# Performance work log

Hardware: AMD Instinct MI355X
Metric: run time of the kernel (lower is better)

Reference implementation:

```python
import jax, jax.numpy as jnp
import numpy as np

B, L, C = 4, 2048, 1024
H = 16
D = C // H
MAX_SCALE_MUL = float(np.log(100.0))


def setup_inputs() -> dict:
    key = jax.random.key(0)
    ks = jax.random.split(key, 4)
    x = jax.random.normal(ks[0], (B, L, C), dtype=jnp.float32)
    attn_bias = jnp.zeros((1, 1, L, L), dtype=jnp.float32)
    qkv_w = jax.random.normal(ks[1], (3 * C, C), dtype=jnp.float32) * (C ** -0.5)
    q_bias = jnp.zeros((C,), dtype=jnp.float32)
    v_bias = jnp.zeros((C,), dtype=jnp.float32)
    scale_mul = jnp.full((1, H, 1, 1), np.log(4.0), dtype=jnp.float32)
    proj_w = jax.random.normal(ks[2], (C, C), dtype=jnp.float32) * (C ** -0.5)
    proj_b = jnp.zeros((C,), dtype=jnp.float32)
    return {"x": x, "attn_bias": attn_bias, "qkv_w": qkv_w, "q_bias": q_bias,
            "v_bias": v_bias, "scale_mul": scale_mul, "proj_w": proj_w, "proj_b": proj_b}


def _l2norm(t, eps=1e-12):
    # matches F.normalize(dim=-1): x / max(||x||, eps)
    n = jnp.sqrt(jnp.sum(t * t, axis=-1, keepdims=True))
    return t / jnp.maximum(n, eps)


def reference(x, attn_bias, qkv_w, q_bias, v_bias, scale_mul, proj_w, proj_b):
    zero_k_bias = jnp.zeros_like(q_bias)
    bias = jnp.concatenate([q_bias, zero_k_bias, v_bias])  # [3C]
    qkv = jnp.einsum('blc,oc->blo', x, qkv_w) + bias        # [B,L,3C]
    qkv = qkv.reshape(B, L, 3, H, D).transpose(2, 0, 3, 1, 4)  # [3,B,H,L,D]
    q, k, v = qkv[0], qkv[1], qkv[2]
    sm = jnp.exp(jnp.minimum(scale_mul, MAX_SCALE_MUL))     # [1,H,1,1]
    q = _l2norm(q) * sm
    k = _l2norm(k)
    scores = jnp.einsum('bhqd,bhkd->bhqk', q, k) * 1.0      # scale=1.0 (l2-norm path)
    scores = scores + attn_bias
    probs = jax.nn.softmax(scores, axis=-1)
    out = jnp.einsum('bhqk,bhkd->bhqd', probs, v)           # [B,H,L,D]
    out = out.transpose(0, 2, 1, 3).reshape(B, L, C)
    return jnp.einsum('blc,oc->blo', out, proj_w) + proj_b
```

## Files before the change

### kernel.cpp

```cpp
#include <hip/hip_runtime.h>
#include <cstdint>


typedef __bf16 bfx8 __attribute__((ext_vector_type(8)));
typedef __bf16 bfx4 __attribute__((ext_vector_type(4)));
typedef float  f32x4 __attribute__((ext_vector_type(4)));

#define NB   4
#define NH   16
#define SEQ  2048
#define CH   1024
#define DD   64
#define MROWS (NB*SEQ)
#define BHLD  (NB*NH*SEQ*DD)
#define LOG2E 1.44269504088896340736f

__device__ __forceinline__ void async16(void* lds, const void* g) {
  __builtin_amdgcn_global_load_lds((const __attribute__((address_space(1))) void*)g,
                                   (__attribute__((address_space(3))) void*)lds, 16, 0, 0);
}
__device__ __forceinline__ f32x4 mfma16(bfx8 a, bfx8 b, f32x4 c) {
  return __builtin_amdgcn_mfma_f32_16x16x32_bf16(a, b, c, 0, 0, 0);
}

extern "C" __device__ float __ocml_exp2_f32(float);
__device__ __forceinline__ float fexp2(float x) {
#if __has_builtin(__builtin_amdgcn_exp2f)
  return __builtin_amdgcn_exp2f(x);
#else
  return __ocml_exp2_f32(x);
#endif
}

__global__ __launch_bounds__(256) void cast_kernel(const float4* __restrict__ src,
                                                   __bf16* __restrict__ dst, int n4) {
  int i = blockIdx.x * 256 + threadIdx.x;
  if (i >= n4) return;
  float4 v = src[i];
  float vv[4] = {v.x, v.y, v.z, v.w};
  bfx4 h;
  #pragma unroll
  for (int j = 0; j < 4; ++j) h[j] = (__bf16)vv[j];
  *(bfx4*)(dst + 4*(size_t)i) = h;
}

__global__ __launch_bounds__(256) void split_kernel(const float4* __restrict__ src,
                                                    __bf16* __restrict__ hi,
                                                    __bf16* __restrict__ lo, int n4) {
  int i = blockIdx.x * 256 + threadIdx.x;
  if (i >= n4) return;
  float4 v = src[i];
  float vv[4] = {v.x, v.y, v.z, v.w};
  bfx4 h, l;
  #pragma unroll
  for (int j = 0; j < 4; ++j) {
    __bf16 hb = (__bf16)vv[j];
    h[j] = hb;
    l[j] = (__bf16)(vv[j] - (float)hb);
  }
  *(bfx4*)(hi + 4*(size_t)i) = h;
  *(bfx4*)(lo + 4*(size_t)i) = l;
}

__global__ __launch_bounds__(256) void scan_nz(const uint4* __restrict__ p, int n4,
                                               int* __restrict__ flag) {
  unsigned acc = 0;
  const int stride = gridDim.x * 256;
  for (int i = blockIdx.x * 256 + threadIdx.x; i < n4; i += stride) {
    uint4 u = p[i];
    acc |= (u.x | u.y | u.z | u.w) & 0x7fffffffu;
  }
  if (acc) atomicOr(flag, 1);
}

__global__ __launch_bounds__(256, 2) void gemmq(
    const __bf16* __restrict__ Ag, const __bf16* __restrict__ Bg,
    const int Ntiles, const int K,
    const float* __restrict__ biasA, const float* __restrict__ biasB,
    const float* __restrict__ scale_mul,
    __bf16* __restrict__ outQ, __bf16* __restrict__ outV)
{
  __shared__ alignas(16) char lds[16384];
  const int tid = threadIdx.x;
  const int lane = tid & 63, w = tid >> 6;
  const int l15 = lane & 15, l4 = lane >> 4;
  const int nwg = (int)gridDim.x;
  const int wk = (int)(blockIdx.x & 7) * (nwg >> 3) + (int)(blockIdx.x >> 3);
  const int mt = wk / Ntiles, nt = wk % Ntiles;
  const int m0 = mt * 128, n0 = nt * 128;
  const int wm = (w >> 1) * 64, wn = (w & 1) * 64;

  const f32x4 zz = {0.f, 0.f, 0.f, 0.f};
  f32x4 acc[4][4];
  #pragma unroll
  for (int a = 0; a < 4; ++a)
    #pragma unroll
    for (int b = 0; b < 4; ++b) acc[a][b] = zz;

  int st_row[2], st_c[2], st_lds[2];
  #pragma unroll
  for (int i = 0; i < 2; ++i) {
    const int s = i*256 + tid;
    st_row[i] = s >> 2;
    st_c[i]   = (s & 3) ^ ((st_row[i] >> 1) & 3);
    st_lds[i] = (i*256 + w*64) * 16;
  }

  for (int k0 = 0; k0 < K; k0 += 32) {
    __syncthreads();
    #pragma unroll
    for (int i = 0; i < 2; ++i) {
      const size_t ga = (size_t)(m0 + st_row[i]) * K + (size_t)(k0 + st_c[i]*8);
      const size_t gb = (size_t)(n0 + st_row[i]) * K + (size_t)(k0 + st_c[i]*8);
      async16(lds +        st_lds[i], Ag + ga);
      async16(lds + 8192 + st_lds[i], Bg + gb);
    }
    __syncthreads();

    bfx8 ah[4], bh[4];
    #pragma unroll
    for (int f = 0; f < 4; ++f) {
      const int ra = wm + f*16 + l15;
      ah[f] = *(const bfx8*)(lds + ra*64 + ((l4 ^ ((ra >> 1) & 3)) * 16));
      const int rb = wn + f*16 + l15;
      bh[f] = *(const bfx8*)(lds + 8192 + rb*64 + ((l4 ^ ((rb >> 1) & 3)) * 16));
    }
    __builtin_amdgcn_s_setprio(1);
    #pragma unroll
    for (int mf = 0; mf < 4; ++mf)
      #pragma unroll
      for (int nf = 0; nf < 4; ++nf)
        acc[mf][nf] = mfma16(ah[mf], bh[nf], acc[mf][nf]);
    __builtin_amdgcn_s_setprio(0);
  }

  const int gcb = n0 + wn;
  const int which = gcb >> 10;
  const int hh = (gcb & (CH-1)) >> 6;
  float smul = 1.f;
  if (which == 0) smul = __expf(fminf(scale_mul[hh], 4.605170185988091f)) * LOG2E;
  #pragma unroll
  for (int mf = 0; mf < 4; ++mf)
    #pragma unroll
    for (int rg = 0; rg < 4; ++rg) {
      #pragma unroll
      for (int nf = 0; nf < 4; ++nf) {
        const int gc = gcb + nf*16 + l15;
        acc[mf][nf][rg] += (which == 0) ? biasA[gc]
                         : ((which == 2) ? biasB[gc - 2*CH] : 0.f);
      }
      const int gr = m0 + wm + mf*16 + 4*l4 + rg;
      const int bb = gr >> 11, ll = gr & (SEQ-1);
      float sc = 1.f;
      if (which < 2) {
        float ss = 0.f;
        #pragma unroll
        for (int nf = 0; nf < 4; ++nf) ss += acc[mf][nf][rg] * acc[mf][nf][rg];
        ss += __shfl_xor(ss, 1); ss += __shfl_xor(ss, 2);
        ss += __shfl_xor(ss, 4); ss += __shfl_xor(ss, 8);
        sc = smul / fmaxf(sqrtf(ss), 1e-12f);
      }
      #pragma unroll
      for (int nf = 0; nf < 4; ++nf) {
        const float v = acc[mf][nf][rg] * sc;
        const int dd = nf*16 + l15;
        if (which < 2)
          outQ[(size_t)which*BHLD + ((size_t)((bb*NH + hh)*SEQ) + ll)*DD + dd] = (__bf16)v;
        else
          outV[((size_t)(bb*NH + hh)*DD + dd)*SEQ + ll] = (__bf16)v;
      }
    }
}

__global__ __launch_bounds__(256, 2) void gemm128s(
    const __bf16* __restrict__ Agh, const __bf16* __restrict__ Agl,
    const __bf16* __restrict__ Bgh, const __bf16* __restrict__ Bgl,
    const int Ntiles, const int K,
    const float* __restrict__ biasA, float* __restrict__ outF)
{
  __shared__ alignas(16) char lds[32768];
  const int tid = threadIdx.x;
  const int lane = tid & 63, w = tid >> 6;
  const int l15 = lane & 15, l4 = lane >> 4;
  const int nwg = (int)gridDim.x;
  const int wk = (int)(blockIdx.x & 7) * (nwg >> 3) + (int)(blockIdx.x >> 3);
  const int mt = wk / Ntiles, nt = wk % Ntiles;
  const int m0 = mt * 128, n0 = nt * 128;
  const int wm = (w >> 1) * 64, wn = (w & 1) * 64;

  const f32x4 zz = {0.f, 0.f, 0.f, 0.f};
  f32x4 acc[4][4];
  #pragma unroll
  for (int a = 0; a < 4; ++a)
    #pragma unroll
    for (int b = 0; b < 4; ++b) acc[a][b] = zz;

  int st_row[2], st_c[2], st_lds[2];
  #pragma unroll
  for (int i = 0; i < 2; ++i) {
    const int s = i*256 + tid;
    st_row[i] = s >> 2;
    st_c[i]   = (s & 3) ^ ((st_row[i] >> 1) & 3);
    st_lds[i] = (i*256 + w*64) * 16;
  }

  for (int k0 = 0; k0 < K; k0 += 32) {
    __syncthreads();
    #pragma unroll
    for (int i = 0; i < 2; ++i) {
      const size_t ga = (size_t)(m0 + st_row[i]) * K + (size_t)(k0 + st_c[i]*8);
      const size_t gb = (size_t)(n0 + st_row[i]) * K + (size_t)(k0 + st_c[i]*8);
      async16(lds +         st_lds[i], Agh + ga);
      async16(lds +  8192 + st_lds[i], Agl + ga);
      async16(lds + 16384 + st_lds[i], Bgh + gb);
      async16(lds + 24576 + st_lds[i], Bgl + gb);
    }
    __syncthreads();

    bfx8 ah[4], al[4], bh[4], bl[4];
    #pragma unroll
    for (int f = 0; f < 4; ++f) {
      const int ra = wm + f*16 + l15;
      const int oa = ra*64 + ((l4 ^ ((ra >> 1) & 3)) * 16);
      ah[f] = *(const bfx8*)(lds + oa);
      al[f] = *(const bfx8*)(lds + 8192 + oa);
      const int rb = wn + f*16 + l15;
      const int ob = rb*64 + ((l4 ^ ((rb >> 1) & 3)) * 16);
      bh[f] = *(const bfx8*)(lds + 16384 + ob);
      bl[f] = *(const bfx8*)(lds + 24576 + ob);
    }
    __builtin_amdgcn_s_setprio(1);
    #pragma unroll
    for (int mf = 0; mf < 4; ++mf)
      #pragma unroll
      for (int nf = 0; nf < 4; ++nf) {
        acc[mf][nf] = mfma16(al[mf], bh[nf], acc[mf][nf]);
        acc[mf][nf] = mfma16(ah[mf], bl[nf], acc[mf][nf]);
        acc[mf][nf] = mfma16(ah[mf], bh[nf], acc[mf][nf]);
      }
    __builtin_amdgcn_s_setprio(0);
  }

  #pragma unroll
  for (int mf = 0; mf < 4; ++mf)
    #pragma unroll
    for (int nf = 0; nf < 4; ++nf)
      #pragma unroll
      for (int rg = 0; rg < 4; ++rg) {
        const int gr = m0 + wm + mf*16 + 4*l4 + rg;
        const int gc = n0 + wn + nf*16 + l15;
        outF[(size_t)gr*CH + gc] = acc[mf][nf][rg] + biasA[gc];
      }
}

__global__ __launch_bounds__(256, 2) void attn_kernel(
    const __bf16* __restrict__ qn, const __bf16* __restrict__ kn,
    const __bf16* __restrict__ vtg, const float* __restrict__ scale_mul,
    const float* __restrict__ bias, const int* __restrict__ flag,
    __bf16* __restrict__ ao_hi, __bf16* __restrict__ ao_lo)
{
  __shared__ alignas(16) char Ks[2][8192];
  __shared__ alignas(16) char Vt[2][8192];
  __shared__ alignas(16) char Ps[16384];

  const int tid = threadIdx.x, lane = tid & 63, w = tid >> 6;
  const int l15 = lane & 15, l4 = lane >> 4;
  const int wk = (int)(blockIdx.x & 7) * 128 + (int)(blockIdx.x >> 3);
  const int qt = wk & 15, h = (wk >> 4) & 15, b = wk >> 8;
  const size_t bh = ((size_t)(b*NH + h)) * SEQ * DD;
  const int hasbias = *flag;
  char* Pw = Ps + w*4096;

  const float Mh = __expf(fminf(scale_mul[h], 4.605170185988091f)) * LOG2E * 1.01f;

  bfx8 Qf[2][2];
  const int q0 = qt*128 + w*32;
  #pragma unroll
  for (int mf = 0; mf < 2; ++mf)
    #pragma unroll
    for (int kd = 0; kd < 2; ++kd)
      Qf[mf][kd] = *(const bfx8*)(qn + bh + (size_t)(q0 + mf*16 + l15)*DD + kd*32 + l4*8);

  bfx8 ones;
  #pragma unroll
  for (int j = 0; j < 8; ++j) ones[j] = (__bf16)1.0f;

  const f32x4 zz = {0.f, 0.f, 0.f, 0.f};
  f32x4 O[2][4];
  f32x4 lsum[2] = {zz, zz};
  float m_[2] = {-1e30f, -1e30f}, l_[2] = {0.f, 0.f};
  #pragma unroll
  for (int mf = 0; mf < 2; ++mf)
    #pragma unroll
    for (int nd = 0; nd < 4; ++nd) O[mf][nd] = zz;

  auto stage = [&](int t, int buf) {
    const __bf16* ksrc = kn + bh + (size_t)t*64*DD;
    const __bf16* vsrc = vtg + bh + (size_t)t*64;
    #pragma unroll
    for (int i = 0; i < 2; ++i) {
      const int s = i*256 + tid;
      const int row = s >> 3;
      const int c = (s & 7) ^ (row & 7);
      async16(Ks[buf] + (size_t)(i*256 + w*64)*16, ksrc + (size_t)row*DD + c*8);
      async16(Vt[buf] + (size_t)(i*256 + w*64)*16, vsrc + (size_t)row*SEQ + c*8);
    }
  };

  stage(0, 0);
  asm volatile("s_waitcnt vmcnt(0)" ::: "memory");
  __builtin_amdgcn_s_barrier();

  #pragma unroll 1
  for (int t = 0; t < 32; ++t) {
    const int cur = t & 1;
    if (t + 1 < 32) stage(t + 1, cur ^ 1);

    f32x4 ST[2][4];
    __builtin_amdgcn_s_setprio(1);
    #pragma unroll
    for (int nf = 0; nf < 4; ++nf) {
      const int r = nf*16 + l15;
      const bfx8 K0 = *(const bfx8*)(Ks[cur] + r*128 + ((l4 ^ (r & 7)) * 16));
      const bfx8 K1 = *(const bfx8*)(Ks[cur] + r*128 + (((4 + l4) ^ (r & 7)) * 16));
      #pragma unroll
      for (int mf = 0; mf < 2; ++mf) {
        f32x4 sacc = mfma16(K0, Qf[mf][0], zz);
        ST[mf][nf] = mfma16(K1, Qf[mf][1], sacc);
      }
    }
    __builtin_amdgcn_s_setprio(0);

    if (!hasbias) {
      #pragma unroll
      for (int mf = 0; mf < 2; ++mf) {
        const int row = mf*16 + l15;
        #pragma unroll
        for (int nf = 0; nf < 4; ++nf) {
          bfx4 p4;
          #pragma unroll
          for (int rg = 0; rg < 4; ++rg)
            p4[rg] = (__bf16)fexp2(ST[mf][nf][rg] - Mh);
          const int cpos = (2*nf + (l4 >> 1)) ^ (row & 7);
          *(bfx4*)(Pw + row*128 + cpos*16 + (l4 & 1)*8) = p4;
        }
      }
    } else {
      #pragma unroll
      for (int mf = 0; mf < 2; ++mf) {
        const size_t qg = (size_t)(q0 + mf*16 + l15);
        const float* bp = bias + qg*SEQ + (size_t)t*64;
        #pragma unroll
        for (int nf = 0; nf < 4; ++nf)
          #pragma unroll
          for (int rg = 0; rg < 4; ++rg)
            ST[mf][nf][rg] += bp[nf*16 + 4*l4 + rg] * LOG2E;

        f32x4 mv = ST[mf][0];
        #pragma unroll
        for (int nf = 1; nf < 4; ++nf)
          #pragma unroll
          for (int rg = 0; rg < 4; ++rg) mv[rg] = fmaxf(mv[rg], ST[mf][nf][rg]);
        float mx = fmaxf(fmaxf(mv[0], mv[1]), fmaxf(mv[2], mv[3]));
        mx = fmaxf(mx, __shfl_xor(mx, 16));
        mx = fmaxf(mx, __shfl_xor(mx, 32));
        const bool skip = __all(mx - m_[mf] <= 12.0f) != 0;
        const float mn = skip ? m_[mf] : fmaxf(m_[mf], mx);
        f32x4 sv = zz;
        #pragma unroll
        for (int nf = 0; nf < 4; ++nf)
          #pragma unroll
          for (int rg = 0; rg < 4; ++rg) {
            const float pv = fexp2(ST[mf][nf][rg] - mn);
            ST[mf][nf][rg] = pv;
            sv[rg] += pv;
          }
        float rs = (sv[0] + sv[1]) + (sv[2] + sv[3]);
        rs += __shfl_xor(rs, 16);
        rs += __shfl_xor(rs, 32);
        if (skip) {
          l_[mf] += rs;
        } else {
          const float corr = fexp2(m_[mf] - mn);
          l_[mf] = l_[mf] * corr + rs;
          m_[mf] = mn;
          #pragma unroll
          for (int nd = 0; nd < 4; ++nd)
            #pragma unroll
            for (int rg = 0; rg < 4; ++rg) O[mf][nd][rg] *= corr;
        }
        const int row = mf*16 + l15;
        #pragma unroll
        for (int nf = 0; nf < 4; ++nf) {
          bfx4 p4;
          #pragma unroll
          for (int rg = 0; rg < 4; ++rg) p4[rg] = (__bf16)ST[mf][nf][rg];
          const int cpos = (2*nf + (l4 >> 1)) ^ (row & 7);
          *(bfx4*)(Pw + row*128 + cpos*16 + (l4 & 1)*8) = p4;
        }
      }
    }

    __builtin_amdgcn_s_setprio(1);
    #pragma unroll
    for (int kk = 0; kk < 2; ++kk) {
      bfx8 Pf[2];
      #pragma unroll
      for (int mf = 0; mf < 2; ++mf) {
        const int row = mf*16 + l15;
        Pf[mf] = *(const bfx8*)(Pw + row*128 + (((4*kk + l4) ^ (row & 7)) * 16));
      }
      #pragma unroll
      for (int nd = 0; nd < 4; ++nd) {
        const int dr = nd*16 + l15;
        const bfx8 Vf = *(const bfx8*)(Vt[cur] + dr*128 + (((4*kk + l4) ^ (dr & 7)) * 16));
        #pragma unroll
        for (int mf = 0; mf < 2; ++mf)
          O[mf][nd] = mfma16(Vf, Pf[mf], O[mf][nd]);
      }
      if (!hasbias) {
        lsum[0] = mfma16(ones, Pf[0], lsum[0]);
        lsum[1] = mfma16(ones, Pf[1], lsum[1]);
      }
    }
    __builtin_amdgcn_s_setprio(0);

    asm volatile("s_waitcnt vmcnt(0)" ::: "memory");
    __builtin_amdgcn_s_barrier();
  }

  if (!hasbias) { l_[0] = lsum[0][0]; l_[1] = lsum[1][0]; }

  #pragma unroll
  for (int mf = 0; mf < 2; ++mf) {
    const float inv = 1.f / l_[mf];
    const int qg = q0 + mf*16 + l15;
    #pragma unroll
    for (int nd = 0; nd < 4; ++nd) {
      bfx4 hb, lb;
      #pragma unroll
      for (int rg = 0; rg < 4; ++rg) {
        const float v = O[mf][nd][rg] * inv;
        hb[rg] = (__bf16)v;
        lb[rg] = (__bf16)(v - (float)hb[rg]);
      }
      const size_t idx = ((size_t)(b*SEQ + qg))*CH + h*DD + nd*16 + 4*l4;
      *(bfx4*)(ao_hi + idx) = hb;
      *(bfx4*)(ao_lo + idx) = lb;
    }
  }
}

extern "C" void kernel_launch(void* const* d_in, const int* in_sizes, int n_in,
                              void* d_out, int out_size, void* d_ws, size_t ws_size,
                              hipStream_t stream) {
  const float* x         = (const float*)d_in[0];
  const float* attn_bias = (const float*)d_in[1];
  const float* qkv_w     = (const float*)d_in[2];
  const float* q_bias    = (const float*)d_in[3];
  const float* v_bias    = (const float*)d_in[4];
  const float* scale_mul = (const float*)d_in[5];
  const float* proj_w    = (const float*)d_in[6];
  const float* proj_b    = (const float*)d_in[7];
  float* out = (float*)d_out;

  char* ws = (char*)d_ws;
  size_t off = 0;
  auto alloc = [&](size_t n) { char* p = ws + off; off += (n + 255) & ~(size_t)255; return p; };
  __bf16* x_h  = (__bf16*)alloc((size_t)MROWS*CH*2);
  __bf16* w_h  = (__bf16*)alloc((size_t)3*CH*CH*2);
  __bf16* p_h  = (__bf16*)alloc((size_t)CH*CH*2);
  __bf16* p_l  = (__bf16*)alloc((size_t)CH*CH*2);
  __bf16* qkvn = (__bf16*)alloc((size_t)2*BHLD*2);
  __bf16* vt   = (__bf16*)alloc((size_t)BHLD*2);
  __bf16* ao_h = (__bf16*)alloc((size_t)MROWS*CH*2);
  __bf16* ao_l = (__bf16*)alloc((size_t)MROWS*CH*2);
  int*    flag = (int*)alloc(256);

  cast_kernel<<<MROWS*CH/4/256, 256, 0, stream>>>((const float4*)x, x_h, MROWS*CH/4);
  cast_kernel<<<3*CH*CH/4/256, 256, 0, stream>>>((const float4*)qkv_w, w_h, 3*CH*CH/4);
  split_kernel<<<CH*CH/4/256, 256, 0, stream>>>((const float4*)proj_w, p_h, p_l, CH*CH/4);

  hipMemsetAsync(flag, 0, sizeof(int), stream);
  scan_nz<<<2048, 256, 0, stream>>>((const uint4*)attn_bias, SEQ*SEQ/4, flag);

  gemmq<<<(MROWS/128)*(3*CH/128), 256, 0, stream>>>(
      x_h, w_h, 3*CH/128, CH, q_bias, v_bias, scale_mul, qkvn, vt);

  attn_kernel<<<NB*NH*(SEQ/128), 256, 0, stream>>>(
      qkvn, qkvn + (size_t)BHLD, vt, scale_mul, attn_bias, flag, ao_h, ao_l);

  gemm128s<<<(MROWS/128)*(CH/128), 256, 0, stream>>>(
      ao_h, ao_l, p_h, p_l, CH/128, CH, proj_b, out);
}
```

Before: 272.0 us.

## Switch attention to 32x32x16 MFMA and pass P via permlane swap instead of LDS

Rewrites the attention inner loop to use 32x32x16 bf16 MFMA tiles in place of 16x16x32, so each wave handles its 32 query rows as one tile. The S accumulator layout is rearranged with v_permlane32_swap into the B-operand layout for the PV MFMA, which removes the per-wave LDS round trip for P along with its 16 KB of shared memory. The goal is fewer LDS reads and writes, fewer MFMA issues and better operand reuse. The cost is more accumulator VGPRs and a dependence on the gfx950 permlane32 swap instruction.

```diff
diff --git a/kernel.cpp b/kernel.cpp
--- a/kernel.cpp
+++ b/kernel.cpp
@@ -5,6 +5,7 @@
 typedef __bf16 bfx8 __attribute__((ext_vector_type(8)));
 typedef __bf16 bfx4 __attribute__((ext_vector_type(4)));
 typedef float  f32x4 __attribute__((ext_vector_type(4)));
+typedef float  f32x16 __attribute__((ext_vector_type(16)));
 
 #define NB   4
 #define NH   16
@@ -21,6 +22,9 @@
 }
 __device__ __forceinline__ f32x4 mfma16(bfx8 a, bfx8 b, f32x4 c) {
   return __builtin_amdgcn_mfma_f32_16x16x32_bf16(a, b, c, 0, 0, 0);
+}
+__device__ __forceinline__ f32x16 mfma32(bfx8 a, bfx8 b, f32x16 c) {
+  return __builtin_amdgcn_mfma_f32_32x32x16_bf16(a, b, c, 0, 0, 0);
 }
 
 extern "C" __device__ float __ocml_exp2_f32(float);
@@ -261,38 +265,30 @@
 {
   __shared__ alignas(16) char Ks[2][8192];
   __shared__ alignas(16) char Vt[2][8192];
-  __shared__ alignas(16) char Ps[16384];
 
   const int tid = threadIdx.x, lane = tid & 63, w = tid >> 6;
-  const int l15 = lane & 15, l4 = lane >> 4;
+  const int l31 = lane & 31, l5 = lane >> 5;
   const int wk = (int)(blockIdx.x & 7) * 128 + (int)(blockIdx.x >> 3);
   const int qt = wk & 15, h = (wk >> 4) & 15, b = wk >> 8;
   const size_t bh = ((size_t)(b*NH + h)) * SEQ * DD;
   const int hasbias = *flag;
-  char* Pw = Ps + w*4096;
 
   const float Mh = __expf(fminf(scale_mul[h], 4.605170185988091f)) * LOG2E * 1.01f;
 
-  bfx8 Qf[2][2];
+  bfx8 Qf[4];
   const int q0 = qt*128 + w*32;
   #pragma unroll
-  for (int mf = 0; mf < 2; ++mf)
-    #pragma unroll
-    for (int kd = 0; kd < 2; ++kd)
-      Qf[mf][kd] = *(const bfx8*)(qn + bh + (size_t)(q0 + mf*16 + l15)*DD + kd*32 + l4*8);
+  for (int kd = 0; kd < 4; ++kd)
+    Qf[kd] = *(const bfx8*)(qn + bh + (size_t)(q0 + l31)*DD + kd*16 + l5*8);
 
   bfx8 ones;
   #pragma unroll
   for (int j = 0; j < 8; ++j) ones[j] = (__bf16)1.0f;
 
-  const f32x4 zz = {0.f, 0.f, 0.f, 0.f};
-  f32x4 O[2][4];
-  f32x4 lsum[2] = {zz, zz};
-  float m_[2] = {-1e30f, -1e30f}, l_[2] = {0.f, 0.f};
-  #pragma unroll
-  for (int mf = 0; mf < 2; ++mf)
-    #pragma unroll
-    for (int nd = 0; nd < 4; ++nd) O[mf][nd] = zz;
+  f32x16 O[2], lsum;
+  #pragma unroll
+  for (int r = 0; r < 16; ++r) { O[0][r] = 0.f; O[1][r] = 0.f; lsum[r] = 0.f; }
+  float m_ = -1e30f, l_ = 0.f;
 
   auto stage = [&](int t, int buf) {
     const __bf16* ksrc = kn + bh + (size_t)t*64*DD;
@@ -316,112 +312,109 @@
     const int cur = t & 1;
     if (t + 1 < 32) stage(t + 1, cur ^ 1);
 
-    f32x4 ST[2][4];
+    f32x16 ST[2];
     __builtin_amdgcn_s_setprio(1);
     #pragma unroll
-    for (int nf = 0; nf < 4; ++nf) {
-      const int r = nf*16 + l15;
-      const bfx8 K0 = *(const bfx8*)(Ks[cur] + r*128 + ((l4 ^ (r & 7)) * 16));
-      const bfx8 K1 = *(const bfx8*)(Ks[cur] + r*128 + (((4 + l4) ^ (r & 7)) * 16));
-      #pragma unroll
-      for (int mf = 0; mf < 2; ++mf) {
-        f32x4 sacc = mfma16(K0, Qf[mf][0], zz);
-        ST[mf][nf] = mfma16(K1, Qf[mf][1], sacc);
-      }
+    for (int kb = 0; kb < 2; ++kb) {
+      f32x16 s;
+      #pragma unroll
+      for (int r = 0; r < 16; ++r) s[r] = 0.f;
+      #pragma unroll
+      for (int kd = 0; kd < 4; ++kd) {
+        const int row = kb*32 + l31;
+        const int c = (2*kd + l5) ^ (l31 & 7);
+        const bfx8 Kf = *(const bfx8*)(Ks[cur] + row*128 + c*16);
+        s = mfma32(Kf, Qf[kd], s);
+      }
+      ST[kb] = s;
     }
     __builtin_amdgcn_s_setprio(0);
 
+    unsigned g32[2][4][2];
     if (!hasbias) {
       #pragma unroll
-      for (int mf = 0; mf < 2; ++mf) {
-        const int row = mf*16 + l15;
-        #pragma unroll
-        for (int nf = 0; nf < 4; ++nf) {
-          bfx4 p4;
+      for (int kb = 0; kb < 2; ++kb)
+        #pragma unroll
+        for (int rh = 0; rh < 4; ++rh) {
+          bfx4 g;
           #pragma unroll
-          for (int rg = 0; rg < 4; ++rg)
-            p4[rg] = (__bf16)fexp2(ST[mf][nf][rg] - Mh);
-          const int cpos = (2*nf + (l4 >> 1)) ^ (row & 7);
-          *(bfx4*)(Pw + row*128 + cpos*16 + (l4 & 1)*8) = p4;
+          for (int j = 0; j < 4; ++j)
+            g[j] = (__bf16)fexp2(ST[kb][4*rh + j] - Mh);
+          union { bfx4 b; unsigned u[2]; } cv; cv.b = g;
+          g32[kb][rh][0] = cv.u[0];
+          g32[kb][rh][1] = cv.u[1];
         }
-      }
     } else {
-      #pragma unroll
-      for (int mf = 0; mf < 2; ++mf) {
-        const size_t qg = (size_t)(q0 + mf*16 + l15);
-        const float* bp = bias + qg*SEQ + (size_t)t*64;
-        #pragma unroll
-        for (int nf = 0; nf < 4; ++nf)
+      const float* bp = bias + (size_t)(q0 + l31)*SEQ + (size_t)t*64;
+      float mx = -1e30f;
+      #pragma unroll
+      for (int kb = 0; kb < 2; ++kb)
+        #pragma unroll
+        for (int r = 0; r < 16; ++r) {
+          ST[kb][r] += bp[32*kb + 4*l5 + (r & 3) + 8*(r >> 2)] * LOG2E;
+          mx = fmaxf(mx, ST[kb][r]);
+        }
+      mx = fmaxf(mx, __shfl_xor(mx, 32));
+      const bool skip = __all(mx - m_ <= 12.0f) != 0;
+      const float mn = skip ? m_ : fmaxf(m_, mx);
+      float rs = 0.f;
+      #pragma unroll
+      for (int kb = 0; kb < 2; ++kb)
+        #pragma unroll
+        for (int r = 0; r < 16; ++r) {
+          const float pv = fexp2(ST[kb][r] - mn);
+          ST[kb][r] = pv;
+          rs += pv;
+        }
+      rs += __shfl_xor(rs, 32);
+      if (skip) {
+        l_ += rs;
+      } else {
+        const float corr = fexp2(m_ - mn);
+        l_ = l_ * corr + rs;
+        m_ = mn;
+        #pragma unroll
+        for (int db = 0; db < 2; ++db)
           #pragma unroll
-          for (int rg = 0; rg < 4; ++rg)
-            ST[mf][nf][rg] += bp[nf*16 + 4*l4 + rg] * LOG2E;
-
-        f32x4 mv = ST[mf][0];
-        #pragma unroll
-        for (int nf = 1; nf < 4; ++nf)
+          for (int r = 0; r < 16; ++r) O[db][r] *= corr;
+      }
+      #pragma unroll
+      for (int kb = 0; kb < 2; ++kb)
+        #pragma unroll
+        for (int rh = 0; rh < 4; ++rh) {
+          bfx4 g;
           #pragma unroll
-          for (int rg = 0; rg < 4; ++rg) mv[rg] = fmaxf(mv[rg], ST[mf][nf][rg]);
-        float mx = fmaxf(fmaxf(mv[0], mv[1]), fmaxf(mv[2], mv[3]));
-        mx = fmaxf(mx, __shfl_xor(mx, 16));
-        mx = fmaxf(mx, __shfl_xor(mx, 32));
-        const bool skip = __all(mx - m_[mf] <= 12.0f) != 0;
-        const float mn = skip ? m_[mf] : fmaxf(m_[mf], mx);
-        f32x4 sv = zz;
-        #pragma unroll
-        for (int nf = 0; nf < 4; ++nf)
-          #pragma unroll
-          for (int rg = 0; rg < 4; ++rg) {
-            const float pv = fexp2(ST[mf][nf][rg] - mn);
-            ST[mf][nf][rg] = pv;
-            sv[rg] += pv;
-          }
-        float rs = (sv[0] + sv[1]) + (sv[2] + sv[3]);
-        rs += __shfl_xor(rs, 16);
-        rs += __shfl_xor(rs, 32);
-        if (skip) {
-          l_[mf] += rs;
-        } else {
-          const float corr = fexp2(m_[mf] - mn);
-          l_[mf] = l_[mf] * corr + rs;
-          m_[mf] = mn;
-          #pragma unroll
-          for (int nd = 0; nd < 4; ++nd)
-            #pragma unroll
-            for (int rg = 0; rg < 4; ++rg) O[mf][nd][rg] *= corr;
+          for (int j = 0; j < 4; ++j) g[j] = (__bf16)ST[kb][4*rh + j];
+          union { bfx4 b; unsigned u[2]; } cv; cv.b = g;
+          g32[kb][rh][0] = cv.u[0];
+          g32[kb][rh][1] = cv.u[1];
         }
-        const int row = mf*16 + l15;
-        #pragma unroll
-        for (int nf = 0; nf < 4; ++nf) {
-          bfx4 p4;
-          #pragma unroll
-          for (int rg = 0; rg < 4; ++rg) p4[rg] = (__bf16)ST[mf][nf][rg];
-          const int cpos = (2*nf + (l4 >> 1)) ^ (row & 7);
-          *(bfx4*)(Pw + row*128 + cpos*16 + (l4 & 1)*8) = p4;
-        }
-      }
+    }
+
+    bfx8 Pf[4];
+    #pragma unroll
+    for (int kk = 0; kk < 4; ++kk) {
+      const int kb = kk >> 1, e = (kk & 1) * 2;
+      unsigned u0 = g32[kb][e][0],   u1 = g32[kb][e][1];
+      unsigned v0 = g32[kb][e+1][0], v1 = g32[kb][e+1][1];
+      asm volatile("v_permlane32_swap_b32 %0, %1" : "+v"(u0), "+v"(v0));
+      asm volatile("v_permlane32_swap_b32 %0, %1" : "+v"(u1), "+v"(v1));
+      union { unsigned u[4]; bfx8 bv; } fb;
+      fb.u[0] = u0; fb.u[1] = u1; fb.u[2] = v0; fb.u[3] = v1;
+      Pf[kk] = fb.bv;
     }
 
     __builtin_amdgcn_s_setprio(1);
     #pragma unroll
-    for (int kk = 0; kk < 2; ++kk) {
-      bfx8 Pf[2];
-      #pragma unroll
-      for (int mf = 0; mf < 2; ++mf) {
-        const int row = mf*16 + l15;
-        Pf[mf] = *(const bfx8*)(Pw + row*128 + (((4*kk + l4) ^ (row & 7)) * 16));
-      }
-      #pragma unroll
-      for (int nd = 0; nd < 4; ++nd) {
-        const int dr = nd*16 + l15;
-        const bfx8 Vf = *(const bfx8*)(Vt[cur] + dr*128 + (((4*kk + l4) ^ (dr & 7)) * 16));
-        #pragma unroll
-        for (int mf = 0; mf < 2; ++mf)
-          O[mf][nd] = mfma16(Vf, Pf[mf], O[mf][nd]);
-      }
-      if (!hasbias) {
-        lsum[0] = mfma16(ones, Pf[0], lsum[0]);
-        lsum[1] = mfma16(ones, Pf[1], lsum[1]);
-      }
+    for (int kk = 0; kk < 4; ++kk) {
+      #pragma unroll
+      for (int db = 0; db < 2; ++db) {
+        const int row = db*32 + l31;
+        const int c = (2*kk + l5) ^ (l31 & 7);
+        const bfx8 Vf = *(const bfx8*)(Vt[cur] + row*128 + c*16);
+        O[db] = mfma32(Vf, Pf[kk], O[db]);
+      }
+      if (!hasbias) lsum = mfma32(ones, Pf[kk], lsum);
     }
     __builtin_amdgcn_s_setprio(0);
 
@@ -429,26 +422,25 @@
     __builtin_amdgcn_s_barrier();
   }
 
-  if (!hasbias) { l_[0] = lsum[0][0]; l_[1] = lsum[1][0]; }
-
-  #pragma unroll
-  for (int mf = 0; mf < 2; ++mf) {
-    const float inv = 1.f / l_[mf];
-    const int qg = q0 + mf*16 + l15;
-    #pragma unroll
-    for (int nd = 0; nd < 4; ++nd) {
+  if (!hasbias) l_ = lsum[0];
+
+  const float inv = 1.f / l_;
+  const int qg = q0 + l31;
+  #pragma unroll
+  for (int db = 0; db < 2; ++db)
+    #pragma unroll
+    for (int rq = 0; rq < 4; ++rq) {
       bfx4 hb, lb;
       #pragma unroll
-      for (int rg = 0; rg < 4; ++rg) {
-        const float v = O[mf][nd][rg] * inv;
-        hb[rg] = (__bf16)v;
-        lb[rg] = (__bf16)(v - (float)hb[rg]);
-      }
-      const size_t idx = ((size_t)(b*SEQ + qg))*CH + h*DD + nd*16 + 4*l4;
+      for (int j = 0; j < 4; ++j) {
+        const float v = O[db][4*rq + j] * inv;
+        hb[j] = (__bf16)v;
+        lb[j] = (__bf16)(v - (float)hb[j]);
+      }
+      const size_t idx = ((size_t)(b*SEQ + qg))*CH + h*DD + db*32 + rq*8 + l5*4;
       *(bfx4*)(ao_hi + idx) = hb;
       *(bfx4*)(ao_lo + idx) = lb;
     }
-  }
 }
 
 extern "C" void kernel_launch(void* const* d_in, const int* in_sizes, int n_in,
```

Result: no change. 275.1 us (+1.1%).
